# Performance work log

Measured on AMD Instinct MI355X. Metric: run time of the kernel, lower is better.

## Reference

```python
import jax, jax.numpy as jnp
import numpy as np

H = 8          # num_heads
T = 2          # num_edge_types
NEG_SLOPE = 0.2


def _edge_softmax(scores, dst, num_nodes):
    # softmax over incoming edges of each destination node, per head
    m = jax.ops.segment_max(scores, dst, num_segments=num_nodes)  # [N,H]
    e = jnp.exp(scores - m[dst])                                   # [E,H]
    s = jax.ops.segment_sum(e, dst, num_segments=num_nodes)        # [N,H]
    return e / s[dst]


def setup_inputs() -> dict:
    key = jax.random.key(0)
    ks = jax.random.split(key, 8)
    N, D, E = 50000, 128, 800000
    return {
        "x": jax.random.normal(ks[0], (N, D), dtype=jnp.float32),
        "w_u": jax.random.normal(ks[1], (H * T, D), dtype=jnp.float32) * (1.0 / np.sqrt(D)),
        "b_u": jax.random.normal(ks[2], (H * T,), dtype=jnp.float32) * 0.01,
        "w_v": jax.random.normal(ks[3], (H * T, D), dtype=jnp.float32) * (1.0 / np.sqrt(D)),
        "src_e0": jax.random.randint(ks[4], (E,), 0, N, dtype=jnp.int32),
        "dst_e0": jax.random.randint(ks[5], (E,), 0, N, dtype=jnp.int32),
        "src_e1": jax.random.randint(ks[6], (E,), 0, N, dtype=jnp.int32),
        "dst_e1": jax.random.randint(ks[7], (E,), 0, N, dtype=jnp.int32),
    }


def reference(x, w_u, b_u, w_v, src_e0, dst_e0, src_e1, dst_e1):
    N, D = x.shape
    head_dim = D // H
    scores_u = x @ w_u.T + b_u   # [N, H*T]
    scores_v = x @ w_v.T         # [N, H*T]
    xh = x.reshape(N, head_dim, H)  # matches torch reshape(-1, head_dim, num_heads)
    outs = [x]  # sep=True
    for t, (src, dst) in enumerate([(src_e0, dst_e0), (src_e1, dst_e1)]):
        u = scores_u[:, t * H:(t + 1) * H]
        v = scores_v[:, t * H:(t + 1) * H]
        s = u[src] + v[dst]                         # u_add_v -> [E,H]
        s = jnp.where(s >= 0, s, NEG_SLOPE * s)     # LeakyReLU(0.2)
        p = _edge_softmax(s, dst, N)                # [E,H]
        msg = xh[src] * p[:, None, :]               # u_mul_e -> [E,head_dim,H]
        agg = jax.ops.segment_sum(msg, dst, num_segments=N)  # [N,head_dim,H]
        outs.append(agg.reshape(N, D))
    return jnp.concatenate(outs, axis=-1)  # [N, D*(1+T)]
```

## Files before the change

### kernel.cpp

```cpp
#include <hip/hip_runtime.h>

#define NEG_SLOPE 0.2f
#define RSHIFT 5
#define RW     32
#define MAXNR  1600
#define CHUNKP 4096

__device__ __forceinline__ ushort f2bf(float f) {
    union { float f; unsigned u; } c; c.f = f;
    unsigned u = c.u;
    return (ushort)((u + 0x7fffu + ((u >> 16) & 1u)) >> 16);
}
__device__ __forceinline__ float bflo(unsigned u) { return __uint_as_float(u << 16); }
__device__ __forceinline__ float bfhi(unsigned u) { return __uint_as_float(u & 0xffff0000u); }

__global__ __launch_bounds__(256) void mega_kernel(
    const float* __restrict__ x, const float* __restrict__ wu,
    const float* __restrict__ bu, const float* __restrict__ wv,
    const int* __restrict__ s0, const int* __restrict__ d0,
    const int* __restrict__ s1, const int* __restrict__ d1,
    float* __restrict__ out, ushort* __restrict__ xbf,
    float* __restrict__ su, float* __restrict__ sv,
    int* __restrict__ gcur, unsigned* __restrict__ pairs,
    int N, int E, int nr, int cap, int scoreBlocks, int ppset)
{
    __shared__ __align__(16) float smemf[32 * 132 + 16 * 132];
    int* smi = (int*)smemf;
    float* wlds = smemf;
    float* xtile = smemf + 32 * 132;
    int tid = threadIdx.x;
    int bid = blockIdx.x;

    if (bid < 2 * ppset) {
        int pb = bid;
        int t = pb / ppset, c = pb % ppset;
        const int* ss = t ? s1 : s0;
        const int* dd = t ? d1 : d0;
        int beg = c * CHUNKP, end = min(E, beg + CHUNKP);
        int* lcnt = smi; int* gb = smi + MAXNR; int* lrun = smi + 2 * MAXNR;
        for (int i = tid; i < nr; i += 256) lcnt[i] = 0;
        __syncthreads();
        for (int e = beg + tid; e < end; e += 256)
            atomicAdd(&lcnt[dd[e] >> RSHIFT], 1);
        __syncthreads();
        for (int i = tid; i < nr; i += 256) {
            gb[i] = atomicAdd(&gcur[t * nr + i], lcnt[i]);
            lrun[i] = 0;
        }
        __syncthreads();
        unsigned* pt = pairs + (size_t)t * nr * cap;
        for (int e = beg + tid; e < end; e += 256) {
            int dst = dd[e], src = ss[e];
            int rr = dst >> RSHIFT;
            int pos = atomicAdd(&lrun[rr], 1);
            pt[(size_t)rr * cap + gb[rr] + pos] = ((unsigned)dst << 16) | (unsigned)src;
        }
        return;
    }
    int nb = bid - 2 * ppset;
    int base = nb * 16;
    for (int i = tid; i < 1024; i += 256) {
        int o = i >> 5, k4 = i & 31;
        float4 w = (o < 16) ? ((const float4*)wu)[i] : ((const float4*)wv)[i - 512];
        *(float4*)(wlds + o * 132 + k4 * 4) = w;
    }
    for (int i2 = tid; i2 < 512; i2 += 256) {
        int I = nb * 512 + i2;
        int nl = i2 >> 5, q = i2 & 31;
        int n = base + nl;
        float4 v = make_float4(0.f, 0.f, 0.f, 0.f);
        if (n < N) {
            v = ((const float4*)x)[I];
            ((float4*)out)[(size_t)n * 96 + q] = v;
            ushort4 b;
            b.x = f2bf(v.x); b.y = f2bf(v.y); b.z = f2bf(v.z); b.w = f2bf(v.w);
            *(ushort4*)(xbf + (size_t)I * 4) = b;
        }
        ((float4*)(xtile + nl * 132))[q] = v;
    }
    __syncthreads();
    int o = tid & 15;
    int nl = tid >> 4;
    int n = base + nl;
    if (n >= N) return;
    const float4* xr4 = (const float4*)(xtile + nl * 132);
    const float4* wur4 = (const float4*)(wlds + o * 132);
    const float4* wvr4 = (const float4*)(wlds + (16 + o) * 132);
    float au0 = 0.f, au1 = 0.f, au2 = 0.f, au3 = 0.f;
    float av0 = 0.f, av1 = 0.f, av2 = 0.f, av3 = 0.f;
#pragma unroll
    for (int kk = 0; kk < 32; ++kk) {
        float4 xv = xr4[kk];
        float4 wuv = wur4[kk];
        float4 wvv = wvr4[kk];
        au0 = fmaf(xv.x, wuv.x, au0);  av0 = fmaf(xv.x, wvv.x, av0);
        au1 = fmaf(xv.y, wuv.y, au1);  av1 = fmaf(xv.y, wvv.y, av1);
        au2 = fmaf(xv.z, wuv.z, au2);  av2 = fmaf(xv.z, wvv.z, av2);
        au3 = fmaf(xv.w, wuv.w, au3);  av3 = fmaf(xv.w, wvv.w, av3);
    }
    su[n * 16 + o] = ((au0 + au1) + (au2 + au3)) + bu[o];
    sv[n * 16 + o] = (av0 + av1) + (av2 + av3);
}

__global__ __launch_bounds__(256, 8) void buildagg_kernel(
    const ushort* __restrict__ xbf, const float* __restrict__ su,
    const float* __restrict__ sv, const int* __restrict__ gcur,
    const unsigned* __restrict__ pairs, float* __restrict__ out,
    int N, int E, int nr, int cap)
{
    __shared__ ushort srcs[768];
    __shared__ int offl[33];
    __shared__ int cursor[32];
    __shared__ __align__(16) float ev4[4][512];
    int r = blockIdx.x, t = blockIdx.y, tid = threadIdx.x;
    int m = gcur[t * nr + r];
    if (m > cap) m = cap;
    const unsigned* p = pairs + ((size_t)t * nr + r) * cap;

    if (tid < 32) cursor[tid] = 0;
    __syncthreads();
    for (int i = tid; i < m; i += 256)
        atomicAdd(&cursor[(p[i] >> 16) & (RW - 1)], 1);
    __syncthreads();
    if (tid < 32) {
        int v = cursor[tid];
        int incl = v;
#pragma unroll
        for (int d = 1; d < 32; d <<= 1) {
            int o = __shfl(incl, tid - d);
            if (tid >= d) incl += o;
        }
        offl[tid + 1] = incl;
        if (tid == 0) offl[0] = 0;
        cursor[tid] = incl - v;
    }
    __syncthreads();
    for (int i = tid; i < m; i += 256) {
        unsigned v = p[i];
        int pos = atomicAdd(&cursor[(v >> 16) & (RW - 1)], 1);
        srcs[pos] = (ushort)(v & 0xffffu);
    }
    __syncthreads();

    int wid = tid >> 6, lane = tid & 63;
    int g2 = lane >> 4, q16 = lane & 15;
    int j0 = q16 * 8;
    int eg = lane >> 1;
    int hh = (lane & 1) * 4;
    float* ev = ev4[wid];
    for (int ln = wid; ln < RW; ln += 4) {
        int n = (r << RSHIFT) + ln;
        if (n >= N) break;
        int beg = offl[ln], end = offl[ln + 1];
        float4 vh4 = *(const float4*)(sv + (size_t)n * 16 + t * 8 + hh);
        float a0 = 0.f, a1 = 0.f, a2 = 0.f, a3 = 0.f;
        float a4 = 0.f, a5 = 0.f, a6 = 0.f, a7 = 0.f;
        float4 l4 = make_float4(0.f, 0.f, 0.f, 0.f);
        for (int cbeg = beg; cbeg < end; cbeg += 64) {
            int cnt = min(end - cbeg, 64);
            int gmax = (cnt + 31) >> 5;
            for (int g = 0; g < gmax; ++g) {
                int e = g * 32 + eg;
                bool valid = e < cnt;
                int sidx = srcs[cbeg + (valid ? e : 0)];
                float4 fu = *(const float4*)(su + (size_t)sidx * 16 + t * 8 + hh);
                float sx = fu.x + vh4.x; sx = (sx >= 0.f) ? sx : NEG_SLOPE * sx;
                float sy = fu.y + vh4.y; sy = (sy >= 0.f) ? sy : NEG_SLOPE * sy;
                float sz = fu.z + vh4.z; sz = (sz >= 0.f) ? sz : NEG_SLOPE * sz;
                float sw = fu.w + vh4.w; sw = (sw >= 0.f) ? sw : NEG_SLOPE * sw;
                float4 ee;
                ee.x = valid ? __expf(sx) : 0.f;
                ee.y = valid ? __expf(sy) : 0.f;
                ee.z = valid ? __expf(sz) : 0.f;
                ee.w = valid ? __expf(sw) : 0.f;
                l4.x += ee.x; l4.y += ee.y; l4.z += ee.z; l4.w += ee.w;
                *(float4*)(ev + e * 8 + hh) = ee;
            }
            int quads = (cnt + 3) >> 2;
            for (int i4 = 0; i4 < quads; i4 += 2) {
                int e0 = (i4 << 2) + g2, e1 = e0 + 4;
                int sA = srcs[cbeg + ((e0 < cnt) ? e0 : 0)];
                int sB = srcs[cbeg + ((e1 < cnt) ? e1 : 0)];
                uint4 uA = *(const uint4*)(xbf + (size_t)sA * 128 + j0);
                uint4 uB = *(const uint4*)(xbf + (size_t)sB * 128 + j0);
                float4 pA0 = *(const float4*)(ev + e0 * 8);
                float4 pA1 = *(const float4*)(ev + e0 * 8 + 4);
                float4 pB0 = *(const float4*)(ev + e1 * 8);
                float4 pB1 = *(const float4*)(ev + e1 * 8 + 4);
                a0 = fmaf(bflo(uA.x), pA0.x, a0);
                a1 = fmaf(bfhi(uA.x), pA0.y, a1);
                a2 = fmaf(bflo(uA.y), pA0.z, a2);
                a3 = fmaf(bfhi(uA.y), pA0.w, a3);
                a4 = fmaf(bflo(uA.z), pA1.x, a4);
                a5 = fmaf(bfhi(uA.z), pA1.y, a5);
                a6 = fmaf(bflo(uA.w), pA1.z, a6);
                a7 = fmaf(bfhi(uA.w), pA1.w, a7);
                a0 = fmaf(bflo(uB.x), pB0.x, a0);
                a1 = fmaf(bfhi(uB.x), pB0.y, a1);
                a2 = fmaf(bflo(uB.y), pB0.z, a2);
                a3 = fmaf(bfhi(uB.y), pB0.w, a3);
                a4 = fmaf(bflo(uB.z), pB1.x, a4);
                a5 = fmaf(bfhi(uB.z), pB1.y, a5);
                a6 = fmaf(bflo(uB.w), pB1.z, a6);
                a7 = fmaf(bfhi(uB.w), pB1.w, a7);
            }
        }
        l4.x += __shfl_xor(l4.x, 2);  l4.y += __shfl_xor(l4.y, 2);
        l4.z += __shfl_xor(l4.z, 2);  l4.w += __shfl_xor(l4.w, 2);
        l4.x += __shfl_xor(l4.x, 4);  l4.y += __shfl_xor(l4.y, 4);
        l4.z += __shfl_xor(l4.z, 4);  l4.w += __shfl_xor(l4.w, 4);
        l4.x += __shfl_xor(l4.x, 8);  l4.y += __shfl_xor(l4.y, 8);
        l4.z += __shfl_xor(l4.z, 8);  l4.w += __shfl_xor(l4.w, 8);
        l4.x += __shfl_xor(l4.x, 16); l4.y += __shfl_xor(l4.y, 16);
        l4.z += __shfl_xor(l4.z, 16); l4.w += __shfl_xor(l4.w, 16);
        l4.x += __shfl_xor(l4.x, 32); l4.y += __shfl_xor(l4.y, 32);
        l4.z += __shfl_xor(l4.z, 32); l4.w += __shfl_xor(l4.w, 32);
        float4 invl4;
        invl4.x = (l4.x > 0.f) ? (1.f / l4.x) : 0.f;
        invl4.y = (l4.y > 0.f) ? (1.f / l4.y) : 0.f;
        invl4.z = (l4.z > 0.f) ? (1.f / l4.z) : 0.f;
        invl4.w = (l4.w > 0.f) ? (1.f / l4.w) : 0.f;
        a0 += __shfl_xor(a0, 16); a0 += __shfl_xor(a0, 32);
        a1 += __shfl_xor(a1, 16); a1 += __shfl_xor(a1, 32);
        a2 += __shfl_xor(a2, 16); a2 += __shfl_xor(a2, 32);
        a3 += __shfl_xor(a3, 16); a3 += __shfl_xor(a3, 32);
        a4 += __shfl_xor(a4, 16); a4 += __shfl_xor(a4, 32);
        a5 += __shfl_xor(a5, 16); a5 += __shfl_xor(a5, 32);
        a6 += __shfl_xor(a6, 16); a6 += __shfl_xor(a6, 32);
        a7 += __shfl_xor(a7, 16); a7 += __shfl_xor(a7, 32);
        float ih0 = __shfl(invl4.x, 0);
        float ih1 = __shfl(invl4.y, 0);
        float ih2 = __shfl(invl4.z, 0);
        float ih3 = __shfl(invl4.w, 0);
        float ih4 = __shfl(invl4.x, 1);
        float ih5 = __shfl(invl4.y, 1);
        float ih6 = __shfl(invl4.z, 1);
        float ih7 = __shfl(invl4.w, 1);
        if (g2 == 0) {
            float* op = out + (size_t)n * 384 + 128 + (size_t)t * 128 + j0;
            *(float4*)op       = make_float4(a0 * ih0, a1 * ih1, a2 * ih2, a3 * ih3);
            *(float4*)(op + 4) = make_float4(a4 * ih4, a5 * ih5, a6 * ih6, a7 * ih7);
        }
    }
}

extern "C" void kernel_launch(void* const* d_in, const int* in_sizes, int n_in,
                              void* d_out, int out_size, void* d_ws, size_t ws_size,
                              hipStream_t stream)
{
    const float* x  = (const float*)d_in[0];
    const float* wu = (const float*)d_in[1];
    const float* bu = (const float*)d_in[2];
    const float* wv = (const float*)d_in[3];
    const int* s0 = (const int*)d_in[4];
    const int* d0 = (const int*)d_in[5];
    const int* s1 = (const int*)d_in[6];
    const int* d1 = (const int*)d_in[7];
    float* out = (float*)d_out;
    int N = in_sizes[0] / 128;
    int E = in_sizes[4];

    int nr = ((N - 1) >> RSHIFT) + 1;
    long long mean = (long long)RW * E / N;
    int cap = (int)(mean + mean / 4 + 64);

    char* ws = (char*)d_ws;
    size_t o = 0;
    auto alloc = [&](size_t bytes) -> void* {
        void* p = ws + o;
        o = (o + bytes + 255) & ~(size_t)255;
        return p;
    };
    float* su       = (float*)alloc((size_t)N * 16 * 4);
    float* sv       = (float*)alloc((size_t)N * 16 * 4);
    int* gcur       = (int*)alloc((size_t)2 * nr * 4);
    unsigned* pairs = (unsigned*)alloc((size_t)2 * nr * cap * 4);
    ushort* xbf     = (ushort*)alloc((size_t)N * 128 * 2);

    int scoreBlocks = (N + 15) / 16;
    int ppset       = (E + CHUNKP - 1) / CHUNKP;

    hipMemsetAsync(gcur, 0, (size_t)2 * nr * 4, stream);
    mega_kernel<<<scoreBlocks + 2 * ppset, 256, 0, stream>>>(
        x, wu, bu, wv, s0, d0, s1, d1, out, xbf, su, sv,
        gcur, pairs, N, E, nr, cap, scoreBlocks, ppset);
    buildagg_kernel<<<dim3(nr, 2), 256, 0, stream>>>(
        xbf, su, sv, gcur, pairs, out, N, E, nr, cap);
}
```

Baseline: 250.1 us.

## Split score arrays per edge type, pad weight LDS rows, stage pairs in LDS

Stores the u/v score arrays as separate per-edge-type [N,8] planes instead of interleaved [N,16], so each edge-score gather touches a compact 32-byte row for its type. The projection stage now uses a row stride of 129 floats for the weight tile with scalar LDS reads, meant to cut bank conflicts, but it also collapses to a single serial accumulator chain per output. The aggregation kernel copies its bucket's packed pairs into shared memory once, so the counting and scatter passes no longer read global memory twice. The partition chunk size is doubled, which halves the number of partition blocks and their global atomics but gives less parallelism.

After: 243.7 us. -2.5%, faster.

```diff
diff --git a/kernel.cpp b/kernel.cpp
--- a/kernel.cpp
+++ b/kernel.cpp
@@ -4,7 +4,7 @@
 #define RSHIFT 5
 #define RW     32
 #define MAXNR  1600
-#define CHUNKP 4096
+#define CHUNKP 8192
 
 __device__ __forceinline__ ushort f2bf(float f) {
     union { float f; unsigned u; } c; c.f = f;
@@ -24,10 +24,10 @@
     int* __restrict__ gcur, unsigned* __restrict__ pairs,
     int N, int E, int nr, int cap, int scoreBlocks, int ppset)
 {
-    __shared__ __align__(16) float smemf[32 * 132 + 16 * 132];
+    __shared__ __align__(16) float smemf[32 * 129 + 16 * 132];
     int* smi = (int*)smemf;
     float* wlds = smemf;
-    float* xtile = smemf + 32 * 132;
+    float* xtile = smemf + 32 * 129;
     int tid = threadIdx.x;
     int bid = blockIdx.x;
 
@@ -59,10 +59,9 @@
     }
     int nb = bid - 2 * ppset;
     int base = nb * 16;
-    for (int i = tid; i < 1024; i += 256) {
-        int o = i >> 5, k4 = i & 31;
-        float4 w = (o < 16) ? ((const float4*)wu)[i] : ((const float4*)wv)[i - 512];
-        *(float4*)(wlds + o * 132 + k4 * 4) = w;
+    for (int i = tid; i < 4096; i += 256) {
+        int o = i >> 7, k = i & 127;
+        wlds[o * 129 + k] = (o < 16) ? wu[i] : wv[i - 2048];
     }
     for (int i2 = tid; i2 < 512; i2 += 256) {
         int I = nb * 512 + i2;
@@ -84,22 +83,24 @@
     int n = base + nl;
     if (n >= N) return;
     const float4* xr4 = (const float4*)(xtile + nl * 132);
-    const float4* wur4 = (const float4*)(wlds + o * 132);
-    const float4* wvr4 = (const float4*)(wlds + (16 + o) * 132);
-    float au0 = 0.f, au1 = 0.f, au2 = 0.f, au3 = 0.f;
-    float av0 = 0.f, av1 = 0.f, av2 = 0.f, av3 = 0.f;
+    const float* wur = wlds + o * 129;
+    const float* wvr = wlds + (16 + o) * 129;
+    float au = 0.f, av = 0.f;
 #pragma unroll
     for (int kk = 0; kk < 32; ++kk) {
         float4 xv = xr4[kk];
-        float4 wuv = wur4[kk];
-        float4 wvv = wvr4[kk];
-        au0 = fmaf(xv.x, wuv.x, au0);  av0 = fmaf(xv.x, wvv.x, av0);
-        au1 = fmaf(xv.y, wuv.y, au1);  av1 = fmaf(xv.y, wvv.y, av1);
-        au2 = fmaf(xv.z, wuv.z, au2);  av2 = fmaf(xv.z, wvv.z, av2);
-        au3 = fmaf(xv.w, wuv.w, au3);  av3 = fmaf(xv.w, wvv.w, av3);
-    }
-    su[n * 16 + o] = ((au0 + au1) + (au2 + au3)) + bu[o];
-    sv[n * 16 + o] = (av0 + av1) + (av2 + av3);
+        int k = kk * 4;
+        au = fmaf(xv.x, wur[k],     au);  av = fmaf(xv.x, wvr[k],     av);
+        au = fmaf(xv.y, wur[k + 1], au);  av = fmaf(xv.y, wvr[k + 1], av);
+        au = fmaf(xv.z, wur[k + 2], au);  av = fmaf(xv.z, wvr[k + 2], av);
+        au = fmaf(xv.w, wur[k + 3], au);  av = fmaf(xv.w, wvr[k + 3], av);
+    }
+    float resu = au + bu[o];
+    float resv = av;
+    size_t toff = (o < 8) ? 0 : (size_t)N * 8;
+    int ho = o & 7;
+    su[toff + (size_t)n * 8 + ho] = resu;
+    sv[toff + (size_t)n * 8 + ho] = resv;
 }
 
 __global__ __launch_bounds__(256, 8) void buildagg_kernel(
@@ -116,11 +117,16 @@
     int m = gcur[t * nr + r];
     if (m > cap) m = cap;
     const unsigned* p = pairs + ((size_t)t * nr + r) * cap;
-
+    const float* sut = su + (size_t)t * N * 8;
+    const float* svt = sv + (size_t)t * N * 8;
+
+    unsigned* pl = (unsigned*)ev4;
+    for (int i = tid; i < m; i += 256)
+        pl[i] = p[i];
     if (tid < 32) cursor[tid] = 0;
     __syncthreads();
     for (int i = tid; i < m; i += 256)
-        atomicAdd(&cursor[(p[i] >> 16) & (RW - 1)], 1);
+        atomicAdd(&cursor[(pl[i] >> 16) & (RW - 1)], 1);
     __syncthreads();
     if (tid < 32) {
         int v = cursor[tid];
@@ -136,7 +142,7 @@
     }
     __syncthreads();
     for (int i = tid; i < m; i += 256) {
-        unsigned v = p[i];
+        unsigned v = pl[i];
         int pos = atomicAdd(&cursor[(v >> 16) & (RW - 1)], 1);
         srcs[pos] = (ushort)(v & 0xffffu);
     }
@@ -152,7 +158,7 @@
         int n = (r << RSHIFT) + ln;
         if (n >= N) break;
         int beg = offl[ln], end = offl[ln + 1];
-        float4 vh4 = *(const float4*)(sv + (size_t)n * 16 + t * 8 + hh);
+        float4 vh4 = *(const float4*)(svt + (size_t)n * 8 + hh);
         float a0 = 0.f, a1 = 0.f, a2 = 0.f, a3 = 0.f;
         float a4 = 0.f, a5 = 0.f, a6 = 0.f, a7 = 0.f;
         float4 l4 = make_float4(0.f, 0.f, 0.f, 0.f);
@@ -163,7 +169,7 @@
                 int e = g * 32 + eg;
                 bool valid = e < cnt;
                 int sidx = srcs[cbeg + (valid ? e : 0)];
-                float4 fu = *(const float4*)(su + (size_t)sidx * 16 + t * 8 + hh);
+                float4 fu = *(const float4*)(sut + (size_t)sidx * 8 + hh);
                 float sx = fu.x + vh4.x; sx = (sx >= 0.f) ? sx : NEG_SLOPE * sx;
                 float sy = fu.y + vh4.y; sy = (sy >= 0.f) ? sy : NEG_SLOPE * sy;
                 float sz = fu.z + vh4.z; sz = (sz >= 0.f) ? sz : NEG_SLOPE * sz;
```
